# Performance work log

Hardware: AMD Instinct MI355X
Metric: run time of the kernel (lower is better)

Reference implementation:

```python
import jax, jax.numpy as jnp
import numpy as np


def setup_inputs() -> dict:
    key = jax.random.key(0)
    ks = jax.random.split(key, 8)
    B, C, N = 32, 1024, 512  # N must equal in_dim for the Linear path
    s = 0.02
    return {
        "x": jax.random.normal(ks[0], (B, C, N), dtype=jnp.float32),
        "Wq": jax.random.normal(ks[1], (N, N), dtype=jnp.float32) * s,
        "bq": jax.random.normal(ks[2], (N,), dtype=jnp.float32) * s,
        "Wk": jax.random.normal(ks[3], (N, N), dtype=jnp.float32) * s,
        "bk": jax.random.normal(ks[4], (N,), dtype=jnp.float32) * s,
        "Wv": jax.random.normal(ks[5], (N, N), dtype=jnp.float32) * s,
        "bv": jax.random.normal(ks[6], (N,), dtype=jnp.float32) * s,
        "beta": jax.random.normal(ks[7], (1,), dtype=jnp.float32),
    }


def reference(x, Wq, bq, Wk, bk, Wv, bv, beta):
    # torch Linear applies to the last axis: y = x @ W.T + b
    q = jnp.einsum('bcn,mn->bcm', x, Wq) + bq  # (B, C, N)
    k = jnp.einsum('bcn,mn->bcm', x, Wk) + bk  # (B, C, N)
    v = jnp.einsum('bcn,mn->bcm', x, Wv) + bv  # (B, C, N)
    # energy = bmm(q, k^T) over channel axis -> (B, C, C); NO 1/sqrt(d) scaling
    energy = jnp.einsum('bcn,bdn->bcd', q, k)
    attention = jax.nn.softmax(energy, axis=-1)
    out_x = jnp.einsum('bcd,bdn->bcn', attention, v)  # (B, C, N)
    out = beta * out_x + v  # beta-scaled residual onto the VALUE projection
    return out
```

## Files before the change

kernel.cpp:

```cpp
#include <hip/hip_runtime.h>
#include <hip/hip_bf16.h>

typedef short s8v __attribute__((ext_vector_type(8)));
typedef float f4v __attribute__((ext_vector_type(4)));

#define MFMA_BF16(a, b, c) __builtin_amdgcn_mfma_f32_16x16x32_bf16((a), (b), (c), 0, 0, 0)

#define GLDS16(g, l) __builtin_amdgcn_global_load_lds( \
    (const __attribute__((address_space(1))) void*)(g), \
    (__attribute__((address_space(3))) void*)(l), 16, 0, 0)

__device__ __forceinline__ short f2bf(float f) {
  __hip_bfloat16 h = __float2bfloat16(f);
  return *reinterpret_cast<short*>(&h);
}
__device__ __forceinline__ float bf2f(short s) {
  __hip_bfloat16 h;
  *reinterpret_cast<short*>(&h) = s;
  return __bfloat162float(h);
}

__global__ __launch_bounds__(256) void cvt_kernel(const float* __restrict__ in,
                                                  short* __restrict__ out, int n8) {
  int i = blockIdx.x * 256 + threadIdx.x;
  if (i >= n8) return;
  const float* p = in + (size_t)i * 8;
  float4 a = *(const float4*)p;
  float4 b = *(const float4*)(p + 4);
  s8v o;
  o[0] = f2bf(a.x); o[1] = f2bf(a.y); o[2] = f2bf(a.z); o[3] = f2bf(a.w);
  o[4] = f2bf(b.x); o[5] = f2bf(b.y); o[6] = f2bf(b.z); o[7] = f2bf(b.w);
  *(s8v*)(out + (size_t)i * 8) = o;
}

template<int KSTEPS, int ASTR, int BSTR>
__device__ __forceinline__ void mm_core(const short* __restrict__ Abase,
                                        const short* __restrict__ Bbase,
                                        short* As, short* Bs, f4v (&acc)[4][4]) {
  const int t = threadIdx.x;
  const int lane = t & 63, w = t >> 6;
  const int lr = lane & 15, lg = lane >> 4;
  const int wr = (w >> 1) * 64, wc = (w & 1) * 64;
  const int srcc = ((lane & 7) * 16) ^ ((lane >> 3) << 4);
  const int rstage = w * 32 + (lane >> 3);

  for (int kt = 0; kt < KSTEPS; ++kt) {
    #pragma unroll
    for (int j = 0; j < 4; ++j)
      GLDS16((const char*)(Abase + (size_t)(rstage + j * 8) * ASTR) + kt * 128 + srcc,
             (char*)As + (w * 32 + j * 8) * 128);
    #pragma unroll
    for (int j = 0; j < 4; ++j)
      GLDS16((const char*)(Bbase + (size_t)(rstage + j * 8) * BSTR) + kt * 128 + srcc,
             (char*)Bs + (w * 32 + j * 8) * 128);
    __syncthreads();
    #pragma unroll
    for (int kk = 0; kk < 2; ++kk) {
      s8v af[4], bfr[4];
      #pragma unroll
      for (int mf = 0; mf < 4; ++mf)
        af[mf] = *(const s8v*)((const char*)As + (wr + mf * 16 + lr) * 128 +
                               ((kk * 64 + lg * 16) ^ ((lr & 7) << 4)));
      #pragma unroll
      for (int nf = 0; nf < 4; ++nf)
        bfr[nf] = *(const s8v*)((const char*)Bs + (wc + nf * 16 + lr) * 128 +
                                ((kk * 64 + lg * 16) ^ ((lr & 7) << 4)));
      #pragma unroll
      for (int mf = 0; mf < 4; ++mf)
        #pragma unroll
        for (int nf = 0; nf < 4; ++nf)
          acc[mf][nf] = MFMA_BF16(af[mf], bfr[nf], acc[mf][nf]);
    }
    __syncthreads();
  }
}

__global__ __launch_bounds__(256) void proj_kernel(
    const short* __restrict__ xb, const short* __restrict__ wb,
    const float* __restrict__ bq, const float* __restrict__ bk, const float* __restrict__ bv,
    short* __restrict__ qo, short* __restrict__ ko, short* __restrict__ vo) {
  const int bx = blockIdx.x;
  const int L = (bx & 7) * 384 + (bx >> 3);
  const int cb = L & 3, rb = (L >> 2) & 255, mat = L >> 10;
  const int R0 = rb * 128, C0 = cb * 128;
  const float* bias = (mat == 0) ? bq : (mat == 1) ? bk : bv;
  short* out = (mat == 0) ? qo : (mat == 1) ? ko : vo;

  __shared__ short As[8192], Bs[8192];
  f4v acc[4][4];
  #pragma unroll
  for (int i = 0; i < 4; i++)
    #pragma unroll
    for (int j = 0; j < 4; j++) acc[i][j] = (f4v){0.f, 0.f, 0.f, 0.f};

  mm_core<8, 512, 512>(xb + (size_t)R0 * 512,
                       wb + (size_t)mat * 512 * 512 + (size_t)C0 * 512, As, Bs, acc);

  const int lane = threadIdx.x & 63, w = threadIdx.x >> 6;
  const int lr = lane & 15, lg = lane >> 4;
  const int wr = (w >> 1) * 64, wc = (w & 1) * 64;
  #pragma unroll
  for (int nf = 0; nf < 4; ++nf) {
    int col = C0 + wc + nf * 16 + lr;
    float bb = bias[col];
    #pragma unroll
    for (int mf = 0; mf < 4; ++mf)
      #pragma unroll
      for (int i = 0; i < 4; i++) {
        int row = R0 + wr + mf * 16 + lg * 4 + i;
        out[(size_t)row * 512 + col] = f2bf(acc[mf][nf][i] + bb);
      }
  }
}

__global__ __launch_bounds__(256) void transpose_kernel(const short* __restrict__ v,
                                                        short* __restrict__ vt) {
  const int nb = blockIdx.x;
  const int cbk = blockIdx.y;
  const int b = blockIdx.z;
  __shared__ short tile[64 * 72];
  const int t = threadIdx.x;
  const int r = t >> 2, qd = t & 3;
  const short* src = v + (size_t)(b * 1024 + cbk * 64 + r) * 512 + nb * 64 + qd * 16;
  s8v v0 = *(const s8v*)src;
  s8v v1 = *(const s8v*)(src + 8);
  *(s8v*)&tile[r * 72 + qd * 16] = v0;
  *(s8v*)&tile[r * 72 + qd * 16 + 8] = v1;
  __syncthreads();
  s8v o0, o1;
  #pragma unroll
  for (int j = 0; j < 8; j++) o0[j] = tile[(qd * 16 + j) * 72 + r];
  #pragma unroll
  for (int j = 0; j < 8; j++) o1[j] = tile[(qd * 16 + 8 + j) * 72 + r];
  short* dst = vt + (size_t)(b * 512 + nb * 64 + r) * 1024 + cbk * 64 + qd * 16;
  *(s8v*)dst = o0;
  *(s8v*)(dst + 8) = o1;
}

__global__ __launch_bounds__(256) void qk_kernel(const short* __restrict__ qb,
                                                 const short* __restrict__ kb,
                                                 short* __restrict__ eb) {
  const int bx = blockIdx.x;
  const int L = (bx & 7) * 256 + (bx >> 3);
  const int rb = L & 7, cb = (L >> 3) & 7, b = L >> 6;
  const int R0 = rb * 128, C0 = cb * 128;

  __shared__ short As[8192], Bs[8192];
  f4v acc[4][4];
  #pragma unroll
  for (int i = 0; i < 4; i++)
    #pragma unroll
    for (int j = 0; j < 4; j++) acc[i][j] = (f4v){0.f, 0.f, 0.f, 0.f};

  mm_core<8, 512, 512>(qb + (size_t)(b * 1024 + R0) * 512,
                       kb + (size_t)(b * 1024 + C0) * 512, As, Bs, acc);

  const int lane = threadIdx.x & 63, w = threadIdx.x >> 6;
  const int lr = lane & 15, lg = lane >> 4;
  const int wr = (w >> 1) * 64, wc = (w & 1) * 64;
  #pragma unroll
  for (int nf = 0; nf < 4; ++nf) {
    int col = C0 + wc + nf * 16 + lr;
    #pragma unroll
    for (int mf = 0; mf < 4; ++mf)
      #pragma unroll
      for (int i = 0; i < 4; i++) {
        int row = R0 + wr + mf * 16 + lg * 4 + i;
        eb[(size_t)(b * 1024 + row) * 1024 + col] = f2bf(acc[mf][nf][i]);
      }
  }
}

__global__ __launch_bounds__(256) void softmax_kernel(short* __restrict__ eb) {
  const int row = blockIdx.x * 4 + (threadIdx.x >> 6);
  const int lane = threadIdx.x & 63;
  short* p = eb + (size_t)row * 1024 + lane * 16;
  s8v a = *(const s8v*)p;
  s8v bvv = *(const s8v*)(p + 8);
  float v[16];
  #pragma unroll
  for (int j = 0; j < 8; j++) { v[j] = bf2f(a[j]); v[8 + j] = bf2f(bvv[j]); }
  float m = v[0];
  #pragma unroll
  for (int j = 1; j < 16; j++) m = fmaxf(m, v[j]);
  #pragma unroll
  for (int s = 1; s <= 32; s <<= 1) m = fmaxf(m, __shfl_xor(m, s));
  float l = 0.f;
  #pragma unroll
  for (int j = 0; j < 16; j++) { v[j] = __expf(v[j] - m); l += v[j]; }
  #pragma unroll
  for (int s = 1; s <= 32; s <<= 1) l += __shfl_xor(l, s);
  const float inv = 1.0f / l;
  s8v o0, o1;
  #pragma unroll
  for (int j = 0; j < 8; j++) { o0[j] = f2bf(v[j] * inv); o1[j] = f2bf(v[8 + j] * inv); }
  *(s8v*)p = o0;
  *(s8v*)(p + 8) = o1;
}

__global__ __launch_bounds__(256) void pv_kernel(const short* __restrict__ eb,
                                                 const short* __restrict__ vt,
                                                 const short* __restrict__ vb,
                                                 const float* __restrict__ beta_p,
                                                 float* __restrict__ outp) {
  const int bx = blockIdx.x;
  const int L = (bx & 7) * 128 + (bx >> 3);
  const int cb = L & 3, rb = (L >> 2) & 7, b = L >> 5;
  const int R0 = rb * 128, C0 = cb * 128;

  __shared__ short As[8192], Bs[8192];
  f4v acc[4][4];
  #pragma unroll
  for (int i = 0; i < 4; i++)
    #pragma unroll
    for (int j = 0; j < 4; j++) acc[i][j] = (f4v){0.f, 0.f, 0.f, 0.f};

  mm_core<16, 1024, 1024>(eb + (size_t)(b * 1024 + R0) * 1024,
                          vt + (size_t)(b * 512 + C0) * 1024, As, Bs, acc);

  const float beta = beta_p[0];
  const int lane = threadIdx.x & 63, w = threadIdx.x >> 6;
  const int lr = lane & 15, lg = lane >> 4;
  const int wr = (w >> 1) * 64, wc = (w & 1) * 64;
  #pragma unroll
  for (int nf = 0; nf < 4; ++nf) {
    int col = C0 + wc + nf * 16 + lr;
    #pragma unroll
    for (int mf = 0; mf < 4; ++mf)
      #pragma unroll
      for (int i = 0; i < 4; i++) {
        int row = R0 + wr + mf * 16 + lg * 4 + i;
        float val = beta * acc[mf][nf][i] +
                    bf2f(vb[(size_t)(b * 1024 + row) * 512 + col]);
        outp[(size_t)(b * 1024 + row) * 512 + col] = val;
      }
  }
}

extern "C" void kernel_launch(void* const* d_in, const int* in_sizes, int n_in,
                              void* d_out, int out_size, void* d_ws, size_t ws_size,
                              hipStream_t stream) {
  (void)in_sizes; (void)n_in; (void)out_size; (void)ws_size;
  const float* x = (const float*)d_in[0];
  const float* Wq = (const float*)d_in[1];
  const float* bq = (const float*)d_in[2];
  const float* Wk = (const float*)d_in[3];
  const float* bk = (const float*)d_in[4];
  const float* Wv = (const float*)d_in[5];
  const float* bv = (const float*)d_in[6];
  const float* beta = (const float*)d_in[7];
  float* out = (float*)d_out;

  char* ws = (char*)d_ws;
  short* xb = (short*)(ws);
  short* wb = (short*)(ws + 33554432);
  short* qb = (short*)(ws + 35127296);
  short* kb = (short*)(ws + 68681728);
  short* vb = (short*)(ws + 102236160);
  short* eb = (short*)(ws + 135790592);
  short* vt = xb;

  cvt_kernel<<<8192, 256, 0, stream>>>(x, xb, 2097152);
  cvt_kernel<<<128, 256, 0, stream>>>(Wq, wb, 32768);
  cvt_kernel<<<128, 256, 0, stream>>>(Wk, wb + 262144, 32768);
  cvt_kernel<<<128, 256, 0, stream>>>(Wv, wb + 524288, 32768);
  proj_kernel<<<3072, 256, 0, stream>>>(xb, wb, bq, bk, bv, qb, kb, vb);
  transpose_kernel<<<dim3(8, 16, 32), 256, 0, stream>>>(vb, vt);
  qk_kernel<<<2048, 256, 0, stream>>>(qb, kb, eb);
  softmax_kernel<<<8192, 256, 0, stream>>>(eb);
  pv_kernel<<<1024, 256, 0, stream>>>(eb, vt, vb, beta, out);
}
```

Before: 236.8 us.

## Double-buffer LDS tiles in shared GEMM core to overlap loads with MFMA

The shared mm_core used by the projection, QK and PV kernels now keeps two LDS buffers for the A and B tiles. While MFMAs run on the current buffer, it issues global-to-LDS loads for the next K step, which hides global load latency behind compute. This doubles the per-block LDS footprint from 32 KB to 64 KB, which may cap how many blocks fit on a CU. The loop still relies on one barrier per step to both complete the prefetch and protect the buffer swap.

Measured after the change: 225.8 us. 4.6% less time.

```diff
diff --git a/kernel.cpp b/kernel.cpp
--- a/kernel.cpp
+++ b/kernel.cpp
@@ -36,7 +36,9 @@
 template<int KSTEPS, int ASTR, int BSTR>
 __device__ __forceinline__ void mm_core(const short* __restrict__ Abase,
                                         const short* __restrict__ Bbase,
-                                        short* As, short* Bs, f4v (&acc)[4][4]) {
+                                        short* As0, short* Bs0,
+                                        short* As1, short* Bs1,
+                                        f4v (&acc)[4][4]) {
   const int t = threadIdx.x;
   const int lane = t & 63, w = t >> 6;
   const int lr = lane & 15, lg = lane >> 4;
@@ -44,7 +46,7 @@
   const int srcc = ((lane & 7) * 16) ^ ((lane >> 3) << 4);
   const int rstage = w * 32 + (lane >> 3);
 
-  for (int kt = 0; kt < KSTEPS; ++kt) {
+  auto stage = [&](short* As, short* Bs, int kt) {
     #pragma unroll
     for (int j = 0; j < 4; ++j)
       GLDS16((const char*)(Abase + (size_t)(rstage + j * 8) * ASTR) + kt * 128 + srcc,
@@ -53,17 +55,24 @@
     for (int j = 0; j < 4; ++j)
       GLDS16((const char*)(Bbase + (size_t)(rstage + j * 8) * BSTR) + kt * 128 + srcc,
              (char*)Bs + (w * 32 + j * 8) * 128);
-    __syncthreads();
+  };
+
+  stage(As0, Bs0, 0);
+  __syncthreads();
+  short* Asc = As0; short* Bsc = Bs0;
+  short* Asn = As1; short* Bsn = Bs1;
+  for (int kt = 0; kt < KSTEPS; ++kt) {
+    if (kt + 1 < KSTEPS) stage(Asn, Bsn, kt + 1);
     #pragma unroll
     for (int kk = 0; kk < 2; ++kk) {
       s8v af[4], bfr[4];
       #pragma unroll
       for (int mf = 0; mf < 4; ++mf)
-        af[mf] = *(const s8v*)((const char*)As + (wr + mf * 16 + lr) * 128 +
+        af[mf] = *(const s8v*)((const char*)Asc + (wr + mf * 16 + lr) * 128 +
                                ((kk * 64 + lg * 16) ^ ((lr & 7) << 4)));
       #pragma unroll
       for (int nf = 0; nf < 4; ++nf)
-        bfr[nf] = *(const s8v*)((const char*)Bs + (wc + nf * 16 + lr) * 128 +
+        bfr[nf] = *(const s8v*)((const char*)Bsc + (wc + nf * 16 + lr) * 128 +
                                 ((kk * 64 + lg * 16) ^ ((lr & 7) << 4)));
       #pragma unroll
       for (int mf = 0; mf < 4; ++mf)
@@ -72,6 +81,8 @@
           acc[mf][nf] = MFMA_BF16(af[mf], bfr[nf], acc[mf][nf]);
     }
     __syncthreads();
+    short* ta = Asc; Asc = Asn; Asn = ta;
+    short* tb = Bsc; Bsc = Bsn; Bsn = tb;
   }
 }
 
@@ -86,7 +97,7 @@
   const float* bias = (mat == 0) ? bq : (mat == 1) ? bk : bv;
   short* out = (mat == 0) ? qo : (mat == 1) ? ko : vo;
 
-  __shared__ short As[8192], Bs[8192];
+  __shared__ short As0[8192], Bs0[8192], As1[8192], Bs1[8192];
   f4v acc[4][4];
   #pragma unroll
   for (int i = 0; i < 4; i++)
@@ -94,7 +105,8 @@
     for (int j = 0; j < 4; j++) acc[i][j] = (f4v){0.f, 0.f, 0.f, 0.f};
 
   mm_core<8, 512, 512>(xb + (size_t)R0 * 512,
-                       wb + (size_t)mat * 512 * 512 + (size_t)C0 * 512, As, Bs, acc);
+                       wb + (size_t)mat * 512 * 512 + (size_t)C0 * 512,
+                       As0, Bs0, As1, Bs1, acc);
 
   const int lane = threadIdx.x & 63, w = threadIdx.x >> 6;
   const int lr = lane & 15, lg = lane >> 4;
@@ -145,7 +157,7 @@
   const int rb = L & 7, cb = (L >> 3) & 7, b = L >> 6;
   const int R0 = rb * 128, C0 = cb * 128;
 
-  __shared__ short As[8192], Bs[8192];
+  __shared__ short As0[8192], Bs0[8192], As1[8192], Bs1[8192];
   f4v acc[4][4];
   #pragma unroll
   for (int i = 0; i < 4; i++)
@@ -153,7 +165,8 @@
     for (int j = 0; j < 4; j++) acc[i][j] = (f4v){0.f, 0.f, 0.f, 0.f};
 
   mm_core<8, 512, 512>(qb + (size_t)(b * 1024 + R0) * 512,
-                       kb + (size_t)(b * 1024 + C0) * 512, As, Bs, acc);
+                       kb + (size_t)(b * 1024 + C0) * 512,
+                       As0, Bs0, As1, Bs1, acc);
 
   const int lane = threadIdx.x & 63, w = threadIdx.x >> 6;
   const int lr = lane & 15, lg = lane >> 4;
@@ -208,7 +221,7 @@
   const int cb = L & 3, rb = (L >> 2) & 7, b = L >> 5;
   const int R0 = rb * 128, C0 = cb * 128;
 
-  __shared__ short As[8192], Bs[8192];
+  __shared__ short As0[8192], Bs0[8192], As1[8192], Bs1[8192];
   f4v acc[4][4];
   #pragma unroll
   for (int i = 0; i < 4; i++)
@@ -216,7 +229,8 @@
     for (int j = 0; j < 4; j++) acc[i][j] = (f4v){0.f, 0.f, 0.f, 0.f};
 
   mm_core<16, 1024, 1024>(eb + (size_t)(b * 1024 + R0) * 1024,
-                          vt + (size_t)(b * 512 + C0) * 1024, As, Bs, acc);
+                          vt + (size_t)(b * 512 + C0) * 1024,
+                          As0, Bs0, As1, Bs1, acc);
 
   const float beta = beta_p[0];
   const int lane = threadIdx.x & 63, w = threadIdx.x >> 6;
```

## Use 256x256 double-buffered MFMA tiles with 512 threads for all GEMMs

Applied to the files above, without the earlier changes.

Replaces the 128x128 single-buffered GEMM core with a 256x256 tile computed by 8 waves. It double-buffers LDS through async global-to-LDS loads with explicit vmcnt waits, prefetches two K-steps ahead, and raises wave priority around the MFMA bursts. The larger tiles give more data reuse per byte loaded, and the prefetching overlaps loads with compute. In exchange there are far fewer blocks (256 for pv, against 256 CUs), 128KB of LDS per block, and high register pressure, which could limit occupancy and leave the GPU underfilled.

Result: slower. 255.6 us (+8.0%).

```diff
diff --git a/kernel.cpp b/kernel.cpp
--- a/kernel.cpp
+++ b/kernel.cpp
@@ -33,81 +33,109 @@
   *(s8v*)(out + (size_t)i * 8) = o;
 }
 
-template<int KSTEPS, int ASTR, int BSTR>
-__device__ __forceinline__ void mm_core(const short* __restrict__ Abase,
-                                        const short* __restrict__ Bbase,
-                                        short* As, short* Bs, f4v (&acc)[4][4]) {
+template<int KT, int ASTR, int BSTR>
+__device__ __forceinline__ void mm256_core(const short* __restrict__ Ab,
+                                           const short* __restrict__ Bb,
+                                           short* lds, f4v (&acc)[8][4]) {
   const int t = threadIdx.x;
-  const int lane = t & 63, w = t >> 6;
+  const int lane = t & 63, wv = t >> 6;
+  const int wm = wv >> 2, wn = wv & 3;
   const int lr = lane & 15, lg = lane >> 4;
-  const int wr = (w >> 1) * 64, wc = (w & 1) * 64;
-  const int srcc = ((lane & 7) * 16) ^ ((lane >> 3) << 4);
-  const int rstage = w * 32 + (lane >> 3);
-
-  for (int kt = 0; kt < KSTEPS; ++kt) {
-    #pragma unroll
-    for (int j = 0; j < 4; ++j)
-      GLDS16((const char*)(Abase + (size_t)(rstage + j * 8) * ASTR) + kt * 128 + srcc,
-             (char*)As + (w * 32 + j * 8) * 128);
-    #pragma unroll
-    for (int j = 0; j < 4; ++j)
-      GLDS16((const char*)(Bbase + (size_t)(rstage + j * 8) * BSTR) + kt * 128 + srcc,
-             (char*)Bs + (w * 32 + j * 8) * 128);
-    __syncthreads();
+
+  const int srow = t >> 3;
+  const int scol = (t & 7) * 16;
+  const int sswz = scol ^ ((srow & 7) << 4);
+
+  auto stage = [&](int tt) {
+    short* buf = lds + (tt & 1) * 32768;
+    #pragma unroll
+    for (int m = 0; m < 2; ++m) {
+      const short* src = m ? Bb : Ab;
+      const int str = m ? BSTR : ASTR;
+      #pragma unroll
+      for (int h = 0; h < 2; ++h)
+        #pragma unroll
+        for (int j = 0; j < 2; ++j) {
+          int row = srow + j * 64;
+          GLDS16((const char*)(src + (size_t)(h * 128 + row) * str + tt * 64) + sswz,
+                 (char*)(buf + (m * 2 + h) * 8192) + row * 128 + scol);
+        }
+    }
+  };
+
+  stage(0);
+  stage(1);
+
+  const int bhalf = wn >> 1;
+  const int brow0 = (wn & 1) * 64;
+
+  for (int tt = 0; tt < KT; ++tt) {
+    if (tt + 1 < KT) asm volatile("s_waitcnt vmcnt(8)" ::: "memory");
+    else             asm volatile("s_waitcnt vmcnt(0)" ::: "memory");
+    __builtin_amdgcn_s_barrier();
+    const char* bufA = (const char*)(lds + (tt & 1) * 32768 + wm * 8192);
+    const char* bufB = (const char*)(lds + (tt & 1) * 32768 + (2 + bhalf) * 8192);
     #pragma unroll
     for (int kk = 0; kk < 2; ++kk) {
-      s8v af[4], bfr[4];
-      #pragma unroll
-      for (int mf = 0; mf < 4; ++mf)
-        af[mf] = *(const s8v*)((const char*)As + (wr + mf * 16 + lr) * 128 +
+      s8v af[8], bfr[4];
+      #pragma unroll
+      for (int mf = 0; mf < 8; ++mf)
+        af[mf] = *(const s8v*)(bufA + (mf * 16 + lr) * 128 +
                                ((kk * 64 + lg * 16) ^ ((lr & 7) << 4)));
       #pragma unroll
       for (int nf = 0; nf < 4; ++nf)
-        bfr[nf] = *(const s8v*)((const char*)Bs + (wc + nf * 16 + lr) * 128 +
+        bfr[nf] = *(const s8v*)(bufB + (brow0 + nf * 16 + lr) * 128 +
                                 ((kk * 64 + lg * 16) ^ ((lr & 7) << 4)));
-      #pragma unroll
-      for (int mf = 0; mf < 4; ++mf)
+      if (kk == 1) {
+        asm volatile("s_waitcnt lgkmcnt(0)" ::: "memory");
+        __builtin_amdgcn_s_barrier();
+        if (tt + 2 < KT) stage(tt + 2);
+      }
+      __builtin_amdgcn_s_setprio(1);
+      #pragma unroll
+      for (int mf = 0; mf < 8; ++mf)
         #pragma unroll
         for (int nf = 0; nf < 4; ++nf)
           acc[mf][nf] = MFMA_BF16(af[mf], bfr[nf], acc[mf][nf]);
+      __builtin_amdgcn_s_setprio(0);
     }
-    __syncthreads();
   }
 }
 
-__global__ __launch_bounds__(256) void proj_kernel(
+__global__ __launch_bounds__(512, 2) void proj_kernel(
     const short* __restrict__ xb, const short* __restrict__ wb,
     const float* __restrict__ bq, const float* __restrict__ bk, const float* __restrict__ bv,
     short* __restrict__ qo, short* __restrict__ ko, short* __restrict__ vo) {
   const int bx = blockIdx.x;
-  const int L = (bx & 7) * 384 + (bx >> 3);
-  const int cb = L & 3, rb = (L >> 2) & 255, mat = L >> 10;
-  const int R0 = rb * 128, C0 = cb * 128;
+  const int L = (bx & 7) * 96 + (bx >> 3);
+  const int cb = L & 1, rbm = L >> 1;
+  const int mat = rbm >> 7, rb = rbm & 127;
+  const int R0 = rb * 256, C0 = cb * 256;
   const float* bias = (mat == 0) ? bq : (mat == 1) ? bk : bv;
   short* out = (mat == 0) ? qo : (mat == 1) ? ko : vo;
 
-  __shared__ short As[8192], Bs[8192];
-  f4v acc[4][4];
-  #pragma unroll
-  for (int i = 0; i < 4; i++)
+  __shared__ short lds[65536];
+  f4v acc[8][4];
+  #pragma unroll
+  for (int i = 0; i < 8; i++)
     #pragma unroll
     for (int j = 0; j < 4; j++) acc[i][j] = (f4v){0.f, 0.f, 0.f, 0.f};
 
-  mm_core<8, 512, 512>(xb + (size_t)R0 * 512,
-                       wb + (size_t)mat * 512 * 512 + (size_t)C0 * 512, As, Bs, acc);
-
-  const int lane = threadIdx.x & 63, w = threadIdx.x >> 6;
+  mm256_core<8, 512, 512>(xb + (size_t)R0 * 512,
+                          wb + (size_t)mat * 512 * 512 + (size_t)C0 * 512, lds, acc);
+
+  const int lane = threadIdx.x & 63, wv = threadIdx.x >> 6;
+  const int wm = wv >> 2, wn = wv & 3;
   const int lr = lane & 15, lg = lane >> 4;
-  const int wr = (w >> 1) * 64, wc = (w & 1) * 64;
   #pragma unroll
   for (int nf = 0; nf < 4; ++nf) {
-    int col = C0 + wc + nf * 16 + lr;
+    int col = C0 + wn * 64 + nf * 16 + lr;
     float bb = bias[col];
     #pragma unroll
-    for (int mf = 0; mf < 4; ++mf)
+    for (int mf = 0; mf < 8; ++mf)
       #pragma unroll
       for (int i = 0; i < 4; i++) {
-        int row = R0 + wr + mf * 16 + lg * 4 + i;
+        int row = R0 + wm * 128 + mf * 16 + lg * 4 + i;
         out[(size_t)row * 512 + col] = f2bf(acc[mf][nf][i] + bb);
       }
   }
@@ -137,35 +165,36 @@
   *(s8v*)(dst + 8) = o1;
 }
 
-__global__ __launch_bounds__(256) void qk_kernel(const short* __restrict__ qb,
-                                                 const short* __restrict__ kb,
-                                                 short* __restrict__ eb) {
+__global__ __launch_bounds__(512, 2) void qk_kernel(const short* __restrict__ qb,
+                                                    const short* __restrict__ kb,
+                                                    short* __restrict__ eb) {
   const int bx = blockIdx.x;
-  const int L = (bx & 7) * 256 + (bx >> 3);
-  const int rb = L & 7, cb = (L >> 3) & 7, b = L >> 6;
-  const int R0 = rb * 128, C0 = cb * 128;
-
-  __shared__ short As[8192], Bs[8192];
-  f4v acc[4][4];
-  #pragma unroll
-  for (int i = 0; i < 4; i++)
+  const int L = (bx & 7) * 64 + (bx >> 3);
+  const int cb = L & 3, rbb = L >> 2;
+  const int rb = rbb & 3, b = rbb >> 2;
+  const int R0 = rb * 256, C0 = cb * 256;
+
+  __shared__ short lds[65536];
+  f4v acc[8][4];
+  #pragma unroll
+  for (int i = 0; i < 8; i++)
     #pragma unroll
     for (int j = 0; j < 4; j++) acc[i][j] = (f4v){0.f, 0.f, 0.f, 0.f};
 
-  mm_core<8, 512, 512>(qb + (size_t)(b * 1024 + R0) * 512,
-                       kb + (size_t)(b * 1024 + C0) * 512, As, Bs, acc);
-
-  const int lane = threadIdx.x & 63, w = threadIdx.x >> 6;
+  mm256_core<8, 512, 512>(qb + (size_t)(b * 1024 + R0) * 512,
+                          kb + (size_t)(b * 1024 + C0) * 512, lds, acc);
+
+  const int lane = threadIdx.x & 63, wv = threadIdx.x >> 6;
+  const int wm = wv >> 2, wn = wv & 3;
   const int lr = lane & 15, lg = lane >> 4;
-  const int wr = (w >> 1) * 64, wc = (w & 1) * 64;
   #pragma unroll
   for (int nf = 0; nf < 4; ++nf) {
-    int col = C0 + wc + nf * 16 + lr;
-    #pragma unroll
-    for (int mf = 0; mf < 4; ++mf)
+    int col = C0 + wn * 64 + nf * 16 + lr;
+    #pragma unroll
+    for (int mf = 0; mf < 8; ++mf)
       #pragma unroll
       for (int i = 0; i < 4; i++) {
-        int row = R0 + wr + mf * 16 + lg * 4 + i;
+        int row = R0 + wm * 128 + mf * 16 + lg * 4 + i;
         eb[(size_t)(b * 1024 + row) * 1024 + col] = f2bf(acc[mf][nf][i]);
       }
   }
@@ -198,38 +227,39 @@
   *(s8v*)(p + 8) = o1;
 }
 
-__global__ __launch_bounds__(256) void pv_kernel(const short* __restrict__ eb,
-                                                 const short* __restrict__ vt,
-                                                 const short* __restrict__ vb,
-                                                 const float* __restrict__ beta_p,
-                                                 float* __restrict__ outp) {
+__global__ __launch_bounds__(512, 2) void pv_kernel(const short* __restrict__ eb,
+                                                    const short* __restrict__ vt,
+                                                    const short* __restrict__ vb,
+                                                    const float* __restrict__ beta_p,
+                                                    float* __restrict__ outp) {
   const int bx = blockIdx.x;
-  const int L = (bx & 7) * 128 + (bx >> 3);
-  const int cb = L & 3, rb = (L >> 2) & 7, b = L >> 5;
-  const int R0 = rb * 128, C0 = cb * 128;
-
-  __shared__ short As[8192], Bs[8192];
-  f4v acc[4][4];
-  #pragma unroll
-  for (int i = 0; i < 4; i++)
+  const int L = (bx & 7) * 32 + (bx >> 3);
+  const int cb = L & 1, rbb = L >> 1;
+  const int rb = rbb & 3, b = rbb >> 2;
+  const int R0 = rb * 256, C0 = cb * 256;
+
+  __shared__ short lds[65536];
+  f4v acc[8][4];
+  #pragma unroll
+  for (int i = 0; i < 8; i++)
     #pragma unroll
     for (int j = 0; j < 4; j++) acc[i][j] = (f4v){0.f, 0.f, 0.f, 0.f};
 
-  mm_core<16, 1024, 1024>(eb + (size_t)(b * 1024 + R0) * 1024,
-                          vt + (size_t)(b * 512 + C0) * 1024, As, Bs, acc);
+  mm256_core<16, 1024, 1024>(eb + (size_t)(b * 1024 + R0) * 1024,
+                             vt + (size_t)(b * 512 + C0) * 1024, lds, acc);
 
   const float beta = beta_p[0];
-  const int lane = threadIdx.x & 63, w = threadIdx.x >> 6;
+  const int lane = threadIdx.x & 63, wv = threadIdx.x >> 6;
+  const int wm = wv >> 2, wn = wv & 3;
   const int lr = lane & 15, lg = lane >> 4;
-  const int wr = (w >> 1) * 64, wc = (w & 1) * 64;
   #pragma unroll
   for (int nf = 0; nf < 4; ++nf) {
-    int col = C0 + wc + nf * 16 + lr;
-    #pragma unroll
-    for (int mf = 0; mf < 4; ++mf)
+    int col = C0 + wn * 64 + nf * 16 + lr;
+    #pragma unroll
+    for (int mf = 0; mf < 8; ++mf)
       #pragma unroll
       for (int i = 0; i < 4; i++) {
-        int row = R0 + wr + mf * 16 + lg * 4 + i;
+        int row = R0 + wm * 128 + mf * 16 + lg * 4 + i;
         float val = beta * acc[mf][nf][i] +
                     bf2f(vb[(size_t)(b * 1024 + row) * 512 + col]);
         outp[(size_t)(b * 1024 + row) * 512 + col] = val;
@@ -264,9 +294,9 @@
   cvt_kernel<<<128, 256, 0, stream>>>(Wq, wb, 32768);
   cvt_kernel<<<128, 256, 0, stream>>>(Wk, wb + 262144, 32768);
   cvt_kernel<<<128, 256, 0, stream>>>(Wv, wb + 524288, 32768);
-  proj_kernel<<<3072, 256, 0, stream>>>(xb, wb, bq, bk, bv, qb, kb, vb);
+  proj_kernel<<<768, 512, 0, stream>>>(xb, wb, bq, bk, bv, qb, kb, vb);
   transpose_kernel<<<dim3(8, 16, 32), 256, 0, stream>>>(vb, vt);
-  qk_kernel<<<2048, 256, 0, stream>>>(qb, kb, eb);
+  qk_kernel<<<512, 512, 0, stream>>>(qb, kb, eb);
   softmax_kernel<<<8192, 256, 0, stream>>>(eb);
-  pv_kernel<<<1024, 256, 0, stream>>>(eb, vt, vb, beta, out);
-}
+  pv_kernel<<<256, 512, 0, stream>>>(eb, vt, vb, beta, out);
+}
```
